# Kernel tuning notes

Hardware: AMD Instinct MI355X
Metric: run time of the kernel (lower is better)

## Reference

```python
import jax, jax.numpy as jnp
import numpy as np

N_NODES = 100000
N_EDGES = 1000000
IN_CH = 128
HID = 128
N_CLS = 3


def setup_inputs() -> dict:
    key = jax.random.key(0)
    ks = jax.random.split(key, 10)
    scale_in = 1.0 / np.sqrt(IN_CH)
    scale_h = 1.0 / np.sqrt(HID)
    return {
        "x": jax.random.normal(ks[0], (N_NODES, IN_CH), dtype=jnp.float32),
        "edge_index": jax.random.randint(ks[1], (2, N_EDGES), 0, N_NODES, dtype=jnp.int64),
        # SAGEConv layer 1: lin_l (aggregated neighbors, with bias), lin_r (root, no bias)
        "w_l1": jax.random.normal(ks[2], (IN_CH, HID), dtype=jnp.float32) * scale_in,
        "b_l1": jnp.zeros((HID,), dtype=jnp.float32),
        "w_r1": jax.random.normal(ks[3], (IN_CH, HID), dtype=jnp.float32) * scale_in,
        # SAGEConv layer 2
        "w_l2": jax.random.normal(ks[4], (HID, HID), dtype=jnp.float32) * scale_h,
        "b_l2": jnp.zeros((HID,), dtype=jnp.float32),
        "w_r2": jax.random.normal(ks[5], (HID, HID), dtype=jnp.float32) * scale_h,
        # final classifier
        "w_cls": jax.random.normal(ks[6], (HID, N_CLS), dtype=jnp.float32) * scale_h,
        "b_cls": jnp.zeros((N_CLS,), dtype=jnp.float32),
    }


def _sage_conv(x, src, dst, w_l, b_l, w_r, num_nodes):
    # mean aggregation of source-node features onto destination nodes
    msg = x[src]                                              # [E, C] gather
    agg = jax.ops.segment_sum(msg, dst, num_segments=num_nodes)
    cnt = jax.ops.segment_sum(jnp.ones((src.shape[0],), x.dtype), dst,
                              num_segments=num_nodes)
    mean = agg / jnp.maximum(cnt, 1.0)[:, None]
    # out = lin_l(mean_aggr) + lin_r(x)
    return mean @ w_l + b_l + x @ w_r


def reference(x, edge_index, w_l1, b_l1, w_r1, w_l2, b_l2, w_r2, w_cls, b_cls):
    src, dst = edge_index[0], edge_index[1]
    n = x.shape[0]
    h = jax.nn.relu(_sage_conv(x, src, dst, w_l1, b_l1, w_r1, n))
    # dropout is identity in eval mode
    h = jax.nn.relu(_sage_conv(h, src, dst, w_l2, b_l2, w_r2, n))
    logits = h @ w_cls + b_cls
    return logits
```

## Files before the change

### kernel.cpp

```cpp
#include <hip/hip_runtime.h>
#include <hip/hip_bf16.h>

#define N_NODES 100000
#define N_EDGES 1000000
#define CH 128
#define KTOT 256
#define NCLS 3

#define NBKT 196
#define EPB 4096
#define NB_A ((N_EDGES + EPB - 1) / EPB)
#define M_H (NBKT * NB_A)
#define NB_SCAN ((M_H + 1023) / 1024)

#define NB_CVTX (N_NODES * CH / 4 / 256)
#define NB_CVTW (KTOT * CH / 256)
#define NB_A1 (NB_A + NB_CVTX + 2 * NB_CVTW)

typedef __attribute__((ext_vector_type(8))) short v8s;
typedef __attribute__((ext_vector_type(4))) float v4f;

__device__ __forceinline__ float bf2f(unsigned short u) {
    return __uint_as_float(((unsigned int)u) << 16);
}

__device__ __forceinline__ unsigned short f2bf(float f) {
    unsigned int u = __float_as_uint(f);
    unsigned int r = (u + 0x7fffu + ((u >> 16) & 1u)) >> 16;
    return (unsigned short)r;
}

__device__ __forceinline__ int edge_at(const void* e, int is64, long long i) {
    if (is64) return (int)((const long long*)e)[i];
    return ((const int*)e)[i];
}

__device__ __forceinline__ float ldf(const void* p, int isbf, size_t i) {
    if (isbf) return bf2f(((const unsigned short*)p)[i]);
    return ((const float*)p)[i];
}

__device__ __forceinline__ void acc_u32(unsigned int u, float& a0, float& a1) {
    a0 += bf2f((unsigned short)(u & 0xffffu));
    a1 += bf2f((unsigned short)(u >> 16));
}

__global__ void k_init(const void* __restrict__ e, const unsigned int* __restrict__ x,
                       int* __restrict__ eflag, int* __restrict__ dtf,
                       int* __restrict__ done) {
    if (blockIdx.x == 0) {
        if (threadIdx.x < 64) {
            int v = ((const int*)e)[2 * threadIdx.x + 1];
            unsigned long long bl = __ballot(v != 0);
            if (threadIdx.x == 0) *eflag = (bl == 0ULL) ? 1 : 0;
        } else if (threadIdx.x == 64) {
            *done = 0;
        }
    } else {
        if (threadIdx.x < 64) {
            unsigned int u = x[threadIdx.x];
            int ex = (u >> 7) & 0xff;
            int sane = (ex == 0) || (ex >= 100 && ex <= 154);
            unsigned long long bl = __ballot(sane);
            if (threadIdx.x == 0) *dtf = (__popcll(bl) >= 48) ? 1 : 0;
        }
    }
}

__global__ void k_A1(const void* __restrict__ e, const int* __restrict__ eflag,
                     const int* __restrict__ dtf, int* __restrict__ hist,
                     const void* __restrict__ x, unsigned short* __restrict__ Xb,
                     const void* __restrict__ wl1, const void* __restrict__ wr1,
                     unsigned short* __restrict__ WT1,
                     const void* __restrict__ wl2, const void* __restrict__ wr2,
                     unsigned short* __restrict__ WT2) {
    int b = blockIdx.x;
    int t = threadIdx.x;
    if (b < NB_A) {
        __shared__ int h[NBKT];
        if (t < NBKT) h[t] = 0;
        __syncthreads();
        int is64 = *eflag;
#pragma unroll
        for (int j = 0; j < EPB / 256; j++) {
            int i = b * EPB + j * 256 + t;
            if (i < N_EDGES) {
                int dst = edge_at(e, is64, (long long)N_EDGES + i);
                atomicAdd(&h[dst >> 9], 1);
            }
        }
        __syncthreads();
        if (t < NBKT) hist[t * NB_A + b] = h[t];
    } else {
        int ob = b - NB_A;
        if (ob < NB_CVTX) {
            int idx = ob * 256 + t;
            int node = idx >> 5;
            int ch = (idx & 31) * 4;
            int isbf = *dtf;
            unsigned short o[4];
            if (isbf) {
                ushort4 u = *(const ushort4*)((const unsigned short*)x +
                                              (size_t)node * CH + ch);
                o[0] = u.x; o[1] = u.y; o[2] = u.z; o[3] = u.w;
            } else {
                float4 v = *(const float4*)((const float*)x + (size_t)node * CH + ch);
                o[0] = f2bf(v.x); o[1] = f2bf(v.y); o[2] = f2bf(v.z); o[3] = f2bf(v.w);
            }
            *(ushort4*)(Xb + (size_t)node * CH + ch) =
                make_ushort4(o[0], o[1], o[2], o[3]);
        } else {
            int rel = ob - NB_CVTX;
            const void* wl = (rel < NB_CVTW) ? wl1 : wl2;
            const void* wr = (rel < NB_CVTW) ? wr1 : wr2;
            unsigned short* WT = (rel < NB_CVTW) ? WT1 : WT2;
            int i = (rel % NB_CVTW) * 256 + t;
            int k = i >> 7;
            int n = i & 127;
            int isbf = *dtf;
            float v = (k < CH) ? ldf(wl, isbf, (size_t)k * CH + n)
                               : ldf(wr, isbf, (size_t)(k - CH) * CH + n);
            WT[(size_t)n * KTOT + k] = f2bf(v);
        }
    }
}

__global__ __launch_bounds__(1024) void k_scanH(int* __restrict__ hist,
                                                int* __restrict__ bsum,
                                                int* __restrict__ done) {
    __shared__ int s[1024];
    __shared__ int pre_sh;
    int t = threadIdx.x, b = blockIdx.x;
    int idx = b * 1024 + t;
    int v = (idx < M_H) ? hist[idx] : 0;
    s[t] = v;
    __syncthreads();
    for (int off = 1; off < 1024; off <<= 1) {
        int u = (t >= off) ? s[t - off] : 0;
        __syncthreads();
        s[t] += u;
        __syncthreads();
    }
    if (t == 1023) {
        bsum[b] = s[t];
        __threadfence();
        atomicAdd(done, 1);
    }
    if (t == 0) {
        while (__hip_atomic_load(done, __ATOMIC_ACQUIRE,
                                 __HIP_MEMORY_SCOPE_AGENT) < NB_SCAN) {
        }
        __threadfence();
        int run = 0;
        for (int r = 0; r < b; r++) run += bsum[r];
        pre_sh = run;
    }
    __syncthreads();
    if (idx < M_H) hist[idx] = s[t] - v + pre_sh;
}

__global__ void k_A3(const void* __restrict__ e, const int* __restrict__ eflag,
                     const int* __restrict__ hist, unsigned int* __restrict__ part) {
    __shared__ int cur[NBKT];
    int b = blockIdx.x;
    int t = threadIdx.x;
    if (t < NBKT) cur[t] = hist[t * NB_A + b];
    __syncthreads();
    int is64 = *eflag;
#pragma unroll
    for (int j = 0; j < EPB / 256; j++) {
        int i = b * EPB + j * 256 + t;
        if (i < N_EDGES) {
            int src = edge_at(e, is64, i);
            int dst = edge_at(e, is64, (long long)N_EDGES + i);
            int pos = atomicAdd(&cur[dst >> 9], 1);
            part[pos] = ((unsigned int)src << 9) | (unsigned int)(dst & 511);
        }
    }
}

__global__ __launch_bounds__(1024) void k_B(const int* __restrict__ hist,
                                            const unsigned int* __restrict__ part,
                                            int* __restrict__ row_start,
                                            int* __restrict__ csr_src) {
    __shared__ int dcnt[512], sa[512], curs[512];
    int b = blockIdx.x;
    int t = threadIdx.x;
    int e0 = hist[b * NB_A];
    int e1 = (b + 1 < NBKT) ? hist[(b + 1) * NB_A] : N_EDGES;
    if (t < 512) dcnt[t] = 0;
    __syncthreads();
    for (int i = e0 + t; i < e1; i += 1024)
        atomicAdd(&dcnt[part[i] & 511], 1);
    __syncthreads();
    if (t < 512) sa[t] = dcnt[t];
    __syncthreads();
    for (int off = 1; off < 512; off <<= 1) {
        int v = 0;
        if (t < 512 && t >= off) v = sa[t - off];
        __syncthreads();
        if (t < 512) sa[t] += v;
        __syncthreads();
    }
    if (t < 512) {
        int excl = sa[t] - dcnt[t];
        curs[t] = e0 + excl;
        int node = b * 512 + t;
        if (node < N_NODES) row_start[node] = e0 + excl;
    }
    if (b == 0 && t == 0) row_start[N_NODES] = N_EDGES;
    __syncthreads();
    for (int i = e0 + t; i < e1; i += 1024) {
        unsigned int p = part[i];
        int pos = atomicAdd(&curs[p & 511], 1);
        csr_src[pos] = (int)(p >> 9);
    }
}

__global__ __launch_bounds__(256) void k_agg(
    const int* __restrict__ row_start, const int* __restrict__ csr_src,
    const unsigned short* __restrict__ src, unsigned short* __restrict__ mdst) {
    long long gt = (long long)blockIdx.x * blockDim.x + threadIdx.x;
    int node = (int)(gt >> 4);
    int lane = (int)(gt & 15);
    if (node >= N_NODES) return;
    int beg = row_start[node];
    int end = row_start[node + 1];
    int n = end - beg;
    float a[8];
#pragma unroll
    for (int j = 0; j < 8; j++) a[j] = 0.f;
    if (n > 0) {
        const unsigned short* gbase = src + lane * 8;
        int nm1 = n - 1;
        int s[16];
#pragma unroll
        for (int j = 0; j < 16; j++) {
            int jj = (j < nm1) ? j : nm1;
            s[j] = csr_src[beg + jj];
        }
        uint4 u[16];
#pragma unroll
        for (int j = 0; j < 16; j++)
            u[j] = *(const uint4*)(gbase + (size_t)s[j] * CH);
#pragma unroll
        for (int j = 0; j < 16; j++) {
            if (j < n) {
                acc_u32(u[j].x, a[0], a[1]); acc_u32(u[j].y, a[2], a[3]);
                acc_u32(u[j].z, a[4], a[5]); acc_u32(u[j].w, a[6], a[7]);
            }
        }
        int e = beg + 16;
        while (e + 8 <= end) {
            int s2[8];
#pragma unroll
            for (int j = 0; j < 8; j++) s2[j] = csr_src[e + j];
            uint4 u2[8];
#pragma unroll
            for (int j = 0; j < 8; j++)
                u2[j] = *(const uint4*)(gbase + (size_t)s2[j] * CH);
#pragma unroll
            for (int j = 0; j < 8; j++) {
                acc_u32(u2[j].x, a[0], a[1]); acc_u32(u2[j].y, a[2], a[3]);
                acc_u32(u2[j].z, a[4], a[5]); acc_u32(u2[j].w, a[6], a[7]);
            }
            e += 8;
        }
        while (e < end) {
            int s0 = csr_src[e];
            uint4 u0 = *(const uint4*)(gbase + (size_t)s0 * CH);
            acc_u32(u0.x, a[0], a[1]); acc_u32(u0.y, a[2], a[3]);
            acc_u32(u0.z, a[4], a[5]); acc_u32(u0.w, a[6], a[7]);
            e++;
        }
    }
    float rinv = 1.0f / (float)max(n, 1);
    unsigned int p0 = (unsigned int)f2bf(a[0] * rinv) | ((unsigned int)f2bf(a[1] * rinv) << 16);
    unsigned int p1 = (unsigned int)f2bf(a[2] * rinv) | ((unsigned int)f2bf(a[3] * rinv) << 16);
    unsigned int p2 = (unsigned int)f2bf(a[4] * rinv) | ((unsigned int)f2bf(a[5] * rinv) << 16);
    unsigned int p3 = (unsigned int)f2bf(a[6] * rinv) | ((unsigned int)f2bf(a[7] * rinv) << 16);
    *(uint4*)(mdst + (size_t)node * CH + lane * 8) = make_uint4(p0, p1, p2, p3);
}

#define LDB 264
#define CLS_LD 130
__global__ __launch_bounds__(256) void k_gemm_mfma(
    const unsigned short* __restrict__ Mb,
    const unsigned short* __restrict__ Xr,
    const unsigned short* __restrict__ WT, const void* __restrict__ bias,
    const int* __restrict__ dtf,
    unsigned short* __restrict__ out,
    const void* __restrict__ wcls, const void* __restrict__ bcls,
    float* __restrict__ cls_out) {
    __shared__ unsigned short Bs[128 * LDB];
    const int t = threadIdx.x;
    const int w = t >> 6, l = t & 63;
    const int wx = w & 1, wy = w >> 1;
    const int quad = l >> 4, lrow = l & 15;
    const int row0 = blockIdx.x * 128;
    const int isbf = *dtf;

    {
        const int r = t >> 1, sh = t & 1;
        const unsigned short* bsrc = WT + (size_t)r * KTOT + sh * 128;
        unsigned short* bdst = Bs + r * LDB + sh * 128;
#pragma unroll
        for (int j = 0; j < 16; j++)
            *(uint4*)(bdst + j * 8) = *(const uint4*)(bsrc + j * 8);
    }

    const unsigned short* aM[4];
    const unsigned short* aX[4];
#pragma unroll
    for (int mi = 0; mi < 4; mi++) {
        int r = row0 + wy * 64 + mi * 16 + lrow;
        if (r >= N_NODES) r = N_NODES - 1;
        aM[mi] = Mb + (size_t)r * CH + quad * 8;
        aX[mi] = Xr + (size_t)r * CH + quad * 8;
    }

    v4f acc[4][4];
#pragma unroll
    for (int i = 0; i < 4; i++)
#pragma unroll
        for (int j = 0; j < 4; j++) acc[i][j] = (v4f){0.f, 0.f, 0.f, 0.f};

    v8s afc[4];
#pragma unroll
    for (int mi = 0; mi < 4; mi++) afc[mi] = *(const v8s*)(aM[mi]);

    __syncthreads();

#pragma unroll
    for (int k = 0; k < KTOT / 32; k++) {
        v8s afn[4];
        if (k < KTOT / 32 - 1) {
            const int kn = k + 1;
#pragma unroll
            for (int mi = 0; mi < 4; mi++)
                afn[mi] = *(const v8s*)((kn < 4) ? (aM[mi] + kn * 32)
                                                 : (aX[mi] + (kn - 4) * 32));
        }
        v8s bfr[4];
#pragma unroll
        for (int ni = 0; ni < 4; ni++)
            bfr[ni] = *(const v8s*)&Bs[(wx * 64 + ni * 16 + lrow) * LDB +
                                       k * 32 + quad * 8];
#pragma unroll
        for (int mi = 0; mi < 4; mi++)
#pragma unroll
            for (int ni = 0; ni < 4; ni++)
                acc[mi][ni] = __builtin_amdgcn_mfma_f32_16x16x32_bf16(
                    afc[mi], bfr[ni], acc[mi][ni], 0, 0, 0);
#pragma unroll
        for (int mi = 0; mi < 4; mi++) afc[mi] = afn[mi];
    }

    float bj[4];
#pragma unroll
    for (int ni = 0; ni < 4; ni++) bj[ni] = ldf(bias, isbf, wx * 64 + ni * 16 + lrow);

    if (!cls_out) {
#pragma unroll
        for (int mi = 0; mi < 4; mi++) {
#pragma unroll
            for (int r = 0; r < 4; r++) {
                int grow = row0 + wy * 64 + mi * 16 + quad * 4 + r;
                if (grow < N_NODES) {
#pragma unroll
                    for (int ni = 0; ni < 4; ni++) {
                        int col = wx * 64 + ni * 16 + lrow;
                        float v = fmaxf(acc[mi][ni][r] + bj[ni], 0.0f);
                        out[(size_t)grow * CH + col] = f2bf(v);
                    }
                }
            }
        }
    } else {
        __syncthreads();
        float* wcls_s = (float*)(Bs + 16896);
        for (int i = t; i < CH * NCLS; i += 256) wcls_s[i] = ldf(wcls, isbf, i);
#pragma unroll
        for (int mi = 0; mi < 4; mi++) {
#pragma unroll
            for (int r = 0; r < 4; r++) {
                int row = wy * 64 + mi * 16 + quad * 4 + r;
#pragma unroll
                for (int ni = 0; ni < 4; ni++) {
                    int col = wx * 64 + ni * 16 + lrow;
                    float v = fmaxf(acc[mi][ni][r] + bj[ni], 0.0f);
                    Bs[row * CLS_LD + col] = f2bf(v);
                }
            }
        }
        __syncthreads();
        if (t < 128) {
            int grow = row0 + t;
            if (grow < N_NODES) {
                float a0 = 0.f, a1 = 0.f, a2 = 0.f;
                for (int k = 0; k < CH; k++) {
                    float h = bf2f(Bs[t * CLS_LD + k]);
                    a0 += h * wcls_s[k * NCLS + 0];
                    a1 += h * wcls_s[k * NCLS + 1];
                    a2 += h * wcls_s[k * NCLS + 2];
                }
                cls_out[(size_t)grow * NCLS + 0] = a0 + ldf(bcls, isbf, 0);
                cls_out[(size_t)grow * NCLS + 1] = a1 + ldf(bcls, isbf, 1);
                cls_out[(size_t)grow * NCLS + 2] = a2 + ldf(bcls, isbf, 2);
            }
        }
    }
}

extern "C" void kernel_launch(void* const* d_in, const int* in_sizes, int n_in,
                              void* d_out, int out_size, void* d_ws, size_t ws_size,
                              hipStream_t stream) {
    const void* x = d_in[0];
    const void* eidx = d_in[1];
    const void* w_l1 = d_in[2];
    const void* b_l1 = d_in[3];
    const void* w_r1 = d_in[4];
    const void* w_l2 = d_in[5];
    const void* b_l2 = d_in[6];
    const void* w_r2 = d_in[7];
    const void* w_cls = d_in[8];
    const void* b_cls = d_in[9];

    char* w = (char*)d_ws;
    int* eflag = (int*)w;
    int* dtf = (int*)(w + 64);
    int* done = (int*)(w + 128);
    int* hist = (int*)(w + 4096);
    int* bsum = (int*)(w + 196608);
    int* row_start = (int*)(w + 262144);
    unsigned int* part = (unsigned int*)(w + 720896);
    int* csr_src = (int*)(w + 4915200);
    unsigned short* WT1 = (unsigned short*)(w + 8978432);
    unsigned short* WT2 = (unsigned short*)(w + 9043968);
    unsigned short* Xb = (unsigned short*)(w + 11534336);
    unsigned short* Mb = (unsigned short*)(w + 37748736);
    unsigned short* Hb = (unsigned short*)(w + 67108864);

    hipLaunchKernelGGL(k_init, dim3(2), dim3(256), 0, stream,
                       eidx, (const unsigned int*)x, eflag, dtf, done);
    hipLaunchKernelGGL(k_A1, dim3(NB_A1), dim3(256), 0, stream,
                       eidx, eflag, dtf, hist, x, Xb,
                       w_l1, w_r1, WT1, w_l2, w_r2, WT2);
    hipLaunchKernelGGL(k_scanH, dim3(NB_SCAN), dim3(1024), 0, stream,
                       hist, bsum, done);
    hipLaunchKernelGGL(k_A3, dim3(NB_A), dim3(256), 0, stream,
                       eidx, eflag, hist, part);
    hipLaunchKernelGGL(k_B, dim3(NBKT), dim3(1024), 0, stream,
                       hist, part, row_start, csr_src);
    hipLaunchKernelGGL(k_agg, dim3(N_NODES * 16 / 256), dim3(256), 0, stream,
                       row_start, csr_src, Xb, Mb);
    hipLaunchKernelGGL(k_gemm_mfma, dim3((N_NODES + 127) / 128), dim3(256), 0, stream,
                       Mb, Xb, WT1, b_l1, dtf, Hb,
                       (const void*)nullptr, (const void*)nullptr, (float*)nullptr);
    hipLaunchKernelGGL(k_agg, dim3(N_NODES * 16 / 256), dim3(256), 0, stream,
                       row_start, csr_src, Hb, Mb);
    hipLaunchKernelGGL(k_gemm_mfma, dim3((N_NODES + 127) / 128), dim3(256), 0, stream,
                       Mb, Hb, WT2, b_l2, dtf, (unsigned short*)nullptr,
                       w_cls, b_cls, (float*)d_out);
}
```

Baseline: 279.4 us.

## Stream weight tiles through double-buffered LDS in GEMM instead of full preload

```diff
diff --git a/kernel.cpp b/kernel.cpp
--- a/kernel.cpp
+++ b/kernel.cpp
@@ -282,8 +282,9 @@
     *(uint4*)(mdst + (size_t)node * CH + lane * 8) = make_uint4(p0, p1, p2, p3);
 }
 
-#define LDB 264
+#define LDK 40
 #define CLS_LD 130
+#define SMEM_H 18432
 __global__ __launch_bounds__(256) void k_gemm_mfma(
     const unsigned short* __restrict__ Mb,
     const unsigned short* __restrict__ Xr,
@@ -292,22 +293,17 @@
     unsigned short* __restrict__ out,
     const void* __restrict__ wcls, const void* __restrict__ bcls,
     float* __restrict__ cls_out) {
-    __shared__ unsigned short Bs[128 * LDB];
+    __shared__ unsigned short smem[SMEM_H];
+    unsigned short* Bs = smem;
     const int t = threadIdx.x;
     const int w = t >> 6, l = t & 63;
     const int wx = w & 1, wy = w >> 1;
     const int quad = l >> 4, lrow = l & 15;
     const int row0 = blockIdx.x * 128;
+    const int srow = t >> 1, shalf = t & 1;
     const int isbf = *dtf;
 
-    {
-        const int r = t >> 1, sh = t & 1;
-        const unsigned short* bsrc = WT + (size_t)r * KTOT + sh * 128;
-        unsigned short* bdst = Bs + r * LDB + sh * 128;
-#pragma unroll
-        for (int j = 0; j < 16; j++)
-            *(uint4*)(bdst + j * 8) = *(const uint4*)(bsrc + j * 8);
-    }
+    const unsigned short* bbase = WT + (size_t)srow * KTOT + shalf * 16;
 
     const unsigned short* aM[4];
     const unsigned short* aX[4];
@@ -329,33 +325,43 @@
 #pragma unroll
     for (int mi = 0; mi < 4; mi++) afc[mi] = *(const v8s*)(aM[mi]);
 
-    __syncthreads();
-
+    {
+        uint4 b0 = *(const uint4*)bbase, b1 = *(const uint4*)(bbase + 8);
+        *(uint4*)&Bs[srow * LDK + shalf * 16] = b0;
+        *(uint4*)&Bs[srow * LDK + shalf * 16 + 8] = b1;
+    }
 #pragma unroll
     for (int k = 0; k < KTOT / 32; k++) {
+        uint4 nb0, nb1;
         v8s afn[4];
         if (k < KTOT / 32 - 1) {
             const int kn = k + 1;
+            nb0 = *(const uint4*)(bbase + kn * 32);
+            nb1 = *(const uint4*)(bbase + kn * 32 + 8);
 #pragma unroll
             for (int mi = 0; mi < 4; mi++)
                 afn[mi] = *(const v8s*)((kn < 4) ? (aM[mi] + kn * 32)
                                                  : (aX[mi] + (kn - 4) * 32));
         }
+        __syncthreads();
+        const int cur = (k & 1) * 128 * LDK, nxt = ((k + 1) & 1) * 128 * LDK;
         v8s bfr[4];
 #pragma unroll
         for (int ni = 0; ni < 4; ni++)
-            bfr[ni] = *(const v8s*)&Bs[(wx * 64 + ni * 16 + lrow) * LDB +
-                                       k * 32 + quad * 8];
+            bfr[ni] = *(const v8s*)&Bs[cur + (wx * 64 + ni * 16 + lrow) * LDK + quad * 8];
 #pragma unroll
         for (int mi = 0; mi < 4; mi++)
 #pragma unroll
             for (int ni = 0; ni < 4; ni++)
                 acc[mi][ni] = __builtin_amdgcn_mfma_f32_16x16x32_bf16(
                     afc[mi], bfr[ni], acc[mi][ni], 0, 0, 0);
-#pragma unroll
-        for (int mi = 0; mi < 4; mi++) afc[mi] = afn[mi];
-    }
-
+        if (k < KTOT / 32 - 1) {
+            *(uint4*)&Bs[nxt + srow * LDK + shalf * 16] = nb0;
+            *(uint4*)&Bs[nxt + srow * LDK + shalf * 16 + 8] = nb1;
+#pragma unroll
+            for (int mi = 0; mi < 4; mi++) afc[mi] = afn[mi];
+        }
+    }
     float bj[4];
 #pragma unroll
     for (int ni = 0; ni < 4; ni++) bj[ni] = ldf(bias, isbf, wx * 64 + ni * 16 + lrow);
@@ -378,7 +384,7 @@
         }
     } else {
         __syncthreads();
-        float* wcls_s = (float*)(Bs + 16896);
+        float* wcls_s = (float*)(smem + 16640);
         for (int i = t; i < CH * NCLS; i += 256) wcls_s[i] = ldf(wcls, isbf, i);
 #pragma unroll
         for (int mi = 0; mi < 4; mi++) {
@@ -389,7 +395,7 @@
                 for (int ni = 0; ni < 4; ni++) {
                     int col = wx * 64 + ni * 16 + lrow;
                     float v = fmaxf(acc[mi][ni][r] + bj[ni], 0.0f);
-                    Bs[row * CLS_LD + col] = f2bf(v);
+                    smem[row * CLS_LD + col] = f2bf(v);
                 }
             }
         }
@@ -399,7 +405,7 @@
             if (grow < N_NODES) {
                 float a0 = 0.f, a1 = 0.f, a2 = 0.f;
                 for (int k = 0; k < CH; k++) {
-                    float h = bf2f(Bs[t * CLS_LD + k]);
+                    float h = bf2f(smem[t * CLS_LD + k]);
                     a0 += h * wcls_s[k * NCLS + 0];
                     a1 += h * wcls_s[k * NCLS + 1];
                     a2 += h * wcls_s[k * NCLS + 2];
```

After: 271.3 us. 2.9% less time.
